# Optimization experiments

Hardware: AMD Instinct MI355X
Metric: run time of the kernel (lower is better)

Reference implementation:

```python
import jax, jax.numpy as jnp
import numpy as np

L, B, T, C, H, V = 12, 4, 1024, 768, 12, 50257
D = C // H
SCALE = 1.0 / float(np.sqrt(D))
EPS = 1e-5


def layernorm(x, g, b):
    m = jnp.mean(x, axis=-1, keepdims=True)
    v = jnp.var(x, axis=-1, keepdims=True)
    return (x - m) / jnp.sqrt(v + EPS) * g + b


def setup_inputs() -> dict:
    key = jax.random.key(0)
    ks = jax.random.split(key, 12)
    w = lambda k, shape: jax.random.normal(k, shape, jnp.float32) * 0.02
    return {
        "idx": jax.random.randint(ks[0], (B, T), 0, V),
        "tok_emb": w(ks[1], (V, C)),
        "pos_emb": w(ks[2], (1, T, C)),
        # per-layer stacked params (leading dim L); Linear stored [in, out]
        "wq": w(ks[3], (L, C, C)), "bq": jnp.zeros((L, C)),
        "wk": w(ks[4], (L, C, C)), "bk": jnp.zeros((L, C)),
        "wv": w(ks[5], (L, C, C)), "bv": jnp.zeros((L, C)),
        "wo": w(ks[6], (L, C, C)), "bo": jnp.zeros((L, C)),
        "ln1_g": jnp.ones((L, C)), "ln1_b": jnp.zeros((L, C)),
        "ln2_g": jnp.ones((L, C)), "ln2_b": jnp.zeros((L, C)),
        "w1": w(ks[7], (L, C, 4 * C)), "b1": jnp.zeros((L, 4 * C)),
        "w2": w(ks[8], (L, 4 * C, C)), "b2": jnp.zeros((L, C)),
        "lnf_g": jnp.ones((C,)), "lnf_b": jnp.zeros((C,)),
        "head_w": w(ks[9], (C, V)),
    }


def gpt_forward(idx, tok_emb, pos_emb, wq, bq, wk, bk, wv, bv, wo, bo,
                ln1_g, ln1_b, ln2_g, ln2_b, w1, b1, w2, b2,
                lnf_g, lnf_b, head_w):
    t = idx.shape[1]
    x = tok_emb[idx] + pos_emb[:, :t, :]                     # [B,T,C]
    mask = jnp.tril(jnp.ones((t, t), dtype=bool))            # causal

    def block(x, p):
        (pwq, pbq, pwk, pbk, pwv, pbv, pwo, pbo,
         g1, be1, g2, be2, pw1, pb1, pw2, pb2) = p
        h = layernorm(x, g1, be1)
        q = (h @ pwq + pbq).reshape(B, t, H, D)
        k = (h @ pwk + pbk).reshape(B, t, H, D)
        v = (h @ pwv + pbv).reshape(B, t, H, D)
        att = jnp.einsum('bthd,bshd->bhts', q, k) * SCALE    # [B,H,T,T]
        att = jnp.where(mask, att, -jnp.inf)
        att = jax.nn.softmax(att, axis=-1)
        y = jnp.einsum('bhts,bshd->bthd', att, v).reshape(B, t, C)
        x = x + y @ pwo + pbo
        h = layernorm(x, g2, be2)
        x = x + jax.nn.gelu(h @ pw1 + pb1, approximate=False) @ pw2 + pb2
        return x, None

    x, _ = jax.lax.scan(block, x, (wq, bq, wk, bk, wv, bv, wo, bo,
                                   ln1_g, ln1_b, ln2_g, ln2_b,
                                   w1, b1, w2, b2))
    x = layernorm(x, lnf_g, lnf_b)
    return x @ head_w                                        # logits [B,T,V]


def reference(idx, tok_emb, pos_emb, wq, bq, wk, bk, wv, bv, wo, bo,
              ln1_g, ln1_b, ln2_g, ln2_b, w1, b1, w2, b2,
              lnf_g, lnf_b, head_w):
    return gpt_forward(idx, tok_emb, pos_emb, wq, bq, wk, bk, wv, bv, wo, bo,
                       ln1_g, ln1_b, ln2_g, ln2_b, w1, b1, w2, b2,
                       lnf_g, lnf_b, head_w)
```

## Files before the change

### kernel.cpp

```cpp
#include <hip/hip_runtime.h>
#include <hip/hip_bf16.h>
#include <math.h>

#define L_ 12
#define B_ 4
#define T_ 1024
#define C_ 768
#define H_ 12
#define D_ 64
#define V_ 50257
#define M_ 4096
#define QKVN 2304
#define FF_ 3072
#define VPAD_ 51200

typedef __hip_bfloat16 bf16;
typedef __attribute__((ext_vector_type(4))) float f32x4;
typedef __attribute__((ext_vector_type(8))) short short8;
typedef __attribute__((ext_vector_type(8))) __bf16 bf16x8;

typedef __attribute__((address_space(1))) void gvoid;
typedef __attribute__((address_space(3))) void svoid;

__device__ __forceinline__ f32x4 mfma_bf16(short8 a, short8 b, f32x4 c) {
  return __builtin_amdgcn_mfma_f32_16x16x32_bf16(
      __builtin_bit_cast(bf16x8, a), __builtin_bit_cast(bf16x8, b), c, 0, 0, 0);
}

__device__ __forceinline__ void gload_lds16(const void* g, void* l) {
  __builtin_amdgcn_global_load_lds((gvoid*)(void*)g, (svoid*)l, 16, 0, 0);
}

__device__ __forceinline__ short f2bf(float x) {
  return __builtin_bit_cast(short, __float2bfloat16(x));
}

__global__ __launch_bounds__(256) void embed_kernel(const int* __restrict__ idx,
    const float* __restrict__ tok, const float* __restrict__ pos, float* __restrict__ x)
{
  const int row = blockIdx.x;
  const int t = row & (T_ - 1);
  const int id = idx[row];
  const float* te = tok + (size_t)id * C_;
  const float* pe = pos + (size_t)t * C_;
  float* xr = x + (size_t)row * C_;
  const int tid = threadIdx.x;
  xr[tid]       = te[tid]       + pe[tid];
  xr[tid + 256] = te[tid + 256] + pe[tid + 256];
  xr[tid + 512] = te[tid + 512] + pe[tid + 512];
}

__global__ __launch_bounds__(256) void ln_kernel(const float* __restrict__ x,
    const float* __restrict__ g, const float* __restrict__ be, bf16* __restrict__ out)
{
  const int row = blockIdx.x;
  const int tid = threadIdx.x;
  const float* xr = x + (size_t)row * C_;
  float v0 = xr[tid], v1 = xr[tid + 256], v2 = xr[tid + 512];
  float s = v0 + v1 + v2;
  float ss = v0 * v0 + v1 * v1 + v2 * v2;
#pragma unroll
  for (int o = 32; o >= 1; o >>= 1) { s += __shfl_xor(s, o, 64); ss += __shfl_xor(ss, o, 64); }
  __shared__ float sm[8];
  const int w = tid >> 6;
  if ((tid & 63) == 0) { sm[w] = s; sm[4 + w] = ss; }
  __syncthreads();
  s = sm[0] + sm[1] + sm[2] + sm[3];
  ss = sm[4] + sm[5] + sm[6] + sm[7];
  const float mean = s * (1.0f / C_);
  const float var = ss * (1.0f / C_) - mean * mean;
  const float rstd = rsqrtf(var + 1e-5f);
  bf16* orow = out + (size_t)row * C_;
  orow[tid]       = __float2bfloat16((v0 - mean) * rstd * g[tid]       + be[tid]);
  orow[tid + 256] = __float2bfloat16((v1 - mean) * rstd * g[tid + 256] + be[tid + 256]);
  orow[tid + 512] = __float2bfloat16((v2 - mean) * rstd * g[tid + 512] + be[tid + 512]);
}

__global__ __launch_bounds__(256) void convt_kernel(const float* __restrict__ in,
    bf16* __restrict__ out, int K, int N, long in_ls, long out_ls, int row_off)
{
  __shared__ float tile[64][65];
  in  += (size_t)blockIdx.z * in_ls;
  out += (size_t)blockIdx.z * out_ls;
  const int k0 = blockIdx.x * 64, n0 = blockIdx.y * 64;
  const int tid = threadIdx.x;
#pragma unroll
  for (int ph = 0; ph < 16; ph++) {
    int e = ph * 256 + tid;
    int lk = e >> 6, ln = e & 63;
    int gn = n0 + ln;
    tile[lk][ln] = (gn < N) ? in[(size_t)(k0 + lk) * N + gn] : 0.0f;
  }
  __syncthreads();
#pragma unroll
  for (int ph = 0; ph < 16; ph++) {
    int e = ph * 256 + tid;
    int lon = e >> 6, lok = e & 63;
    out[(size_t)(row_off + n0 + lon) * K + k0 + lok] = __float2bfloat16(tile[lok][lon]);
  }
}

__global__ __launch_bounds__(256) void packb_kernel(const float* __restrict__ bq,
    const float* __restrict__ bk, const float* __restrict__ bv, float* __restrict__ out)
{
  const int i = blockIdx.x * 256 + threadIdx.x;
  const int ly = i / QKVN, c = i % QKVN;
  float v;
  if (c < C_)            v = bq[ly * C_ + c];
  else if (c < 2 * C_)   v = bk[ly * C_ + c - C_];
  else                   v = bv[ly * C_ + c - 2 * C_];
  out[i] = v;
}

template<bool BIAS, bool GELU, bool RESID, bool BF16OUT>
__global__ __launch_bounds__(256) void gemm_bt(
    const short* __restrict__ A, const short* __restrict__ Bt,
    const float* __restrict__ bias, const float* resid,
    void* out, int M, int N, int K)
{
  __shared__ short As[128 * 64];
  __shared__ short Bs[128 * 64];
  const int tid = threadIdx.x;
  const int w = tid >> 6, l = tid & 63;
  const int l15 = l & 15, l4 = l >> 4;
  const int wr = w >> 1, wc = w & 1;
  const int nwg = gridDim.x * gridDim.y;
  const int id = blockIdx.y * gridDim.x + blockIdx.x;
  const int chunk = nwg >> 3;
  const int swz = (id & 7) * chunk + (id >> 3);
  const long m0 = (long)(swz % gridDim.x) * 128;
  const long n0 = (long)(swz / gridDim.x) * 128;

  f32x4 acc[4][4] = {};
  const int lrow8 = l >> 3;
  const int lc = l & 7;

  for (int kt = 0; kt < K; kt += 64) {
#pragma unroll
    for (int j = 0; j < 8; j++) {
      const int c = w * 8 + j;
      const int isA = (c < 16);
      const int cc = isA ? c : (c - 16);
      const int row = cc * 8 + lrow8;
      const int colsw = ((lc ^ (row & 7)) << 3);
      const short* gp = (isA ? A + (size_t)(m0 + row) * K : Bt + (size_t)(n0 + row) * K) + kt + colsw;
      short* sp = (isA ? As : Bs) + row * 64 + (lc << 3);
      gload_lds16(gp, sp);
    }
    __syncthreads();
#pragma unroll
    for (int ks = 0; ks < 2; ks++) {
      short8 af[4], bfr[4];
#pragma unroll
      for (int i = 0; i < 4; i++) {
        int row = wr * 64 + i * 16 + l15;
        int cs = (ks * 32 + l4 * 8) ^ ((row & 7) << 3);
        af[i] = *(const short8*)&As[row * 64 + cs];
      }
#pragma unroll
      for (int jn = 0; jn < 4; jn++) {
        int row = wc * 64 + jn * 16 + l15;
        int cs = (ks * 32 + l4 * 8) ^ ((row & 7) << 3);
        bfr[jn] = *(const short8*)&Bs[row * 64 + cs];
      }
#pragma unroll
      for (int i = 0; i < 4; i++)
#pragma unroll
        for (int jn = 0; jn < 4; jn++)
          acc[i][jn] = mfma_bf16(af[i], bfr[jn], acc[i][jn]);
    }
    __syncthreads();
  }

#pragma unroll
  for (int i = 0; i < 4; i++) {
    const long rbase = m0 + wr * 64 + i * 16 + l4 * 4;
#pragma unroll
    for (int jn = 0; jn < 4; jn++) {
      const long col = n0 + wc * 64 + jn * 16 + l15;
      const float bv = BIAS ? bias[col] : 0.0f;
#pragma unroll
      for (int r = 0; r < 4; r++) {
        float v = acc[i][jn][r] + bv;
        if (GELU) v = 0.5f * v * (1.0f + erff(v * 0.70710678118654752f));
        const size_t o = (size_t)(rbase + r) * (size_t)N + col;
        if (RESID)        ((float*)out)[o] = resid[o] + v;
        else if (BF16OUT) ((bf16*)out)[o] = __float2bfloat16(v);
        else              ((float*)out)[o] = v;
      }
    }
  }
}

template<bool BIAS, bool GELU, bool RESID, bool BF16OUT>
__global__ __launch_bounds__(256) void gemm64(
    const short* __restrict__ A, const short* __restrict__ Bt,
    const float* __restrict__ bias, const float* resid,
    void* out, int M, int N, int K)
{
  __shared__ short As[64 * 64];
  __shared__ short Bs[128 * 64];
  const int tid = threadIdx.x;
  const int w = tid >> 6, l = tid & 63;
  const int l15 = l & 15, l4 = l >> 4;
  const int wm = w >> 1, wn = w & 1;
  const int nwg = gridDim.x * gridDim.y;
  const int id = blockIdx.y * gridDim.x + blockIdx.x;
  const int chunk = nwg >> 3;
  const int swz = (id & 7) * chunk + (id >> 3);
  const long m0 = (long)(swz % gridDim.x) * 64;
  const long n0 = (long)(swz / gridDim.x) * 128;
  const int rr = tid >> 3, g = tid & 7;

  f32x4 acc[2][4] = {};

  for (int kt = 0; kt < K; kt += 64) {
#pragma unroll
    for (int p = 0; p < 2; p++) {
      const int row = p * 32 + rr;
      const int cg = ((g ^ (row & 7)) << 3);
      gload_lds16(A + (size_t)(m0 + row) * K + kt + cg, &As[row * 64 + g * 8]);
    }
#pragma unroll
    for (int p = 0; p < 4; p++) {
      const int row = p * 32 + rr;
      const int cg = ((g ^ (row & 7)) << 3);
      gload_lds16(Bt + (size_t)(n0 + row) * K + kt + cg, &Bs[row * 64 + g * 8]);
    }
    __syncthreads();
#pragma unroll
    for (int ks = 0; ks < 2; ks++) {
      short8 af[2], bfr[4];
#pragma unroll
      for (int i = 0; i < 2; i++) {
        int row = wm * 32 + i * 16 + l15;
        int cs = (ks * 32 + l4 * 8) ^ ((row & 7) << 3);
        af[i] = *(const short8*)&As[row * 64 + cs];
      }
#pragma unroll
      for (int j = 0; j < 4; j++) {
        int row = wn * 64 + j * 16 + l15;
        int cs = (ks * 32 + l4 * 8) ^ ((row & 7) << 3);
        bfr[j] = *(const short8*)&Bs[row * 64 + cs];
      }
#pragma unroll
      for (int i = 0; i < 2; i++)
#pragma unroll
        for (int j = 0; j < 4; j++)
          acc[i][j] = mfma_bf16(af[i], bfr[j], acc[i][j]);
    }
    __syncthreads();
  }

#pragma unroll
  for (int i = 0; i < 2; i++) {
    const long rbase = m0 + wm * 32 + i * 16 + l4 * 4;
#pragma unroll
    for (int j = 0; j < 4; j++) {
      const long col = n0 + wn * 64 + j * 16 + l15;
      const float bv = BIAS ? bias[col] : 0.0f;
#pragma unroll
      for (int r = 0; r < 4; r++) {
        float v = acc[i][j][r] + bv;
        if (GELU) v = 0.5f * v * (1.0f + erff(v * 0.70710678118654752f));
        const size_t o = (size_t)(rbase + r) * (size_t)N + col;
        if (RESID)        ((float*)out)[o] = resid[o] + v;
        else if (BF16OUT) ((bf16*)out)[o] = __float2bfloat16(v);
        else              ((float*)out)[o] = v;
      }
    }
  }
}

__global__ __launch_bounds__(512, 1) void gemm256(
    const short* __restrict__ A, const short* __restrict__ Bt,
    float* __restrict__ out, int N, int K)
{
  __shared__ short As[2][256 * 64];
  __shared__ short Bs[2][256 * 64];
  const int tid = threadIdx.x;
  const int l = tid & 63, l15 = l & 15, l4 = l >> 4;
  const int wv = tid >> 6, wm = wv >> 2, wn = wv & 3;
  const int bid = blockIdx.x;
  const int x = bid & 7, r = bid >> 3;
  const int mt = (x & 1) * 8 + (r & 7);
  const int nt = (x >> 1) * 50 + (r >> 3);
  const long m0 = (long)mt * 256;
  const long n0 = (long)nt * 256;
  const int nkt = K >> 6;
  const int rr = tid >> 3, g = tid & 7;

  f32x4 acc[8][4] = {};

  auto stA = [&](int s, int kt, int off) {
#pragma unroll
    for (int p = 0; p < 2; p++) {
      const int row = p * 128 + off + rr;
      gload_lds16(A + (size_t)(m0 + row) * K + (kt << 6) + ((g ^ (row & 7)) << 3),
                  &As[s][row * 64 + g * 8]);
    }
  };
  auto stB = [&](int s, int kt, int off) {
#pragma unroll
    for (int p = 0; p < 2; p++) {
      const int row = p * 128 + ((rr >> 5) << 6) + (rr & 31) + off;
      gload_lds16(Bt + (size_t)(n0 + row) * K + (kt << 6) + ((g ^ (row & 7)) << 3),
                  &Bs[s][row * 64 + g * 8]);
    }
  };
  auto rdA = [&](int s, int mf, int ks) {
    const int row = wm * 128 + mf * 16 + l15;
    const int cs = (ks * 32 + l4 * 8) ^ ((row & 7) << 3);
    return *(const short8*)&As[s][row * 64 + cs];
  };
  auto rdB = [&](int s, int nf, int ks) {
    const int row = wn * 64 + nf * 16 + l15;
    const int cs = (ks * 32 + l4 * 8) ^ ((row & 7) << 3);
    return *(const short8*)&Bs[s][row * 64 + cs];
  };

  stA(0, 0, 0); stB(0, 0, 0); stA(0, 0, 64); stB(0, 0, 32);

  int q = 0;
  for (int kt = 0; kt < nkt; ++kt, q ^= 1) {
    const int ktn = (kt + 1 < nkt) ? kt + 1 : kt;
    short8 a0[2][4], a1[2][4], b0[2][2], b1[2][2];

    stA(q ^ 1, ktn, 0);
    asm volatile("s_waitcnt vmcnt(6)" ::: "memory");
    __builtin_amdgcn_s_barrier();
#pragma unroll
    for (int ks = 0; ks < 2; ks++) {
#pragma unroll
      for (int f = 0; f < 4; f++) a0[ks][f] = rdA(q, f, ks);
#pragma unroll
      for (int j = 0; j < 2; j++) b0[ks][j] = rdB(q, j, ks);
    }
    __builtin_amdgcn_s_setprio(1);
#pragma unroll
    for (int f = 0; f < 4; f++)
#pragma unroll
      for (int j = 0; j < 2; j++) {
        acc[f][j] = mfma_bf16(a0[0][f], b0[0][j], acc[f][j]);
        acc[f][j] = mfma_bf16(a0[1][f], b0[1][j], acc[f][j]);
      }
    __builtin_amdgcn_s_setprio(0);

    stB(q ^ 1, ktn, 0);
    asm volatile("s_waitcnt vmcnt(6)" ::: "memory");
    __builtin_amdgcn_s_barrier();
#pragma unroll
    for (int ks = 0; ks < 2; ks++)
#pragma unroll
      for (int f = 0; f < 4; f++) a1[ks][f] = rdA(q, f + 4, ks);
    __builtin_amdgcn_s_setprio(1);
#pragma unroll
    for (int f = 0; f < 4; f++)
#pragma unroll
      for (int j = 0; j < 2; j++) {
        acc[f + 4][j] = mfma_bf16(a1[0][f], b0[0][j], acc[f + 4][j]);
        acc[f + 4][j] = mfma_bf16(a1[1][f], b0[1][j], acc[f + 4][j]);
      }
    __builtin_amdgcn_s_setprio(0);

    stA(q ^ 1, ktn, 64);
    asm volatile("s_waitcnt vmcnt(6)" ::: "memory");
    __builtin_amdgcn_s_barrier();
#pragma unroll
    for (int ks = 0; ks < 2; ks++)
#pragma unroll
      for (int j = 0; j < 2; j++) b1[ks][j] = rdB(q, j + 2, ks);
    __builtin_amdgcn_s_setprio(1);
#pragma unroll
    for (int f = 0; f < 4; f++)
#pragma unroll
      for (int j = 0; j < 2; j++) {
        acc[f][j + 2] = mfma_bf16(a0[0][f], b1[0][j], acc[f][j + 2]);
        acc[f][j + 2] = mfma_bf16(a0[1][f], b1[1][j], acc[f][j + 2]);
      }
    __builtin_amdgcn_s_setprio(0);

    stB(q ^ 1, ktn, 32);
    __builtin_amdgcn_s_setprio(1);
#pragma unroll
    for (int f = 0; f < 4; f++)
#pragma unroll
      for (int j = 0; j < 2; j++) {
        acc[f + 4][j + 2] = mfma_bf16(a1[0][f], b1[0][j], acc[f + 4][j + 2]);
        acc[f + 4][j + 2] = mfma_bf16(a1[1][f], b1[1][j], acc[f + 4][j + 2]);
      }
    __builtin_amdgcn_s_setprio(0);
  }

#pragma unroll
  for (int i = 0; i < 8; i++) {
#pragma unroll
    for (int j = 0; j < 4; j++) {
      const long col = n0 + wn * 64 + j * 16 + l15;
      if (col >= N) continue;
#pragma unroll
      for (int r2 = 0; r2 < 4; r2++) {
        const long row = m0 + wm * 128 + i * 16 + l4 * 4 + r2;
        out[(size_t)row * (size_t)N + col] = acc[i][j][r2];
      }
    }
  }
}

__global__ __launch_bounds__(256) void transv_kernel(const short* __restrict__ qkv,
                                                     short* __restrict__ vt)
{
  __shared__ short tile[64][72];
  const int t0 = blockIdx.x * 64, bh = blockIdx.y;
  const int b = bh / H_, h = bh % H_;
  const int tid = threadIdx.x;
#pragma unroll
  for (int ph = 0; ph < 2; ph++) {
    int lt = ph * 32 + (tid >> 3);
    int ld = (tid & 7) * 8;
    short8 v = *(const short8*)&qkv[(size_t)(b * T_ + t0 + lt) * QKVN + 2 * C_ + h * D_ + ld];
#pragma unroll
    for (int j = 0; j < 8; j++) tile[lt][ld + j] = v[j];
  }
  __syncthreads();
#pragma unroll
  for (int ph = 0; ph < 2; ph++) {
    int ldd = ph * 32 + (tid >> 3);
    int ltt = (tid & 7) * 8;
    short8 v;
#pragma unroll
    for (int j = 0; j < 8; j++) v[j] = tile[ltt + j][ldd];
    *(short8*)&vt[((size_t)bh * D_ + ldd) * T_ + t0 + ltt] = v;
  }
}

__global__ __launch_bounds__(256) void attn_kernel(const short* __restrict__ qkv,
    const short* __restrict__ vt, bf16* __restrict__ y)
{
  __shared__ short Ks[2][64 * 64];
  __shared__ short Vs[2][64 * 64];
  const int qt = (gridDim.x - 1) - blockIdx.x;
  const int bh = blockIdx.y;
  const int b = bh / H_, h = bh % H_;
  const int tid = threadIdx.x, w = tid >> 6, l = tid & 63;
  const int l15 = l & 15, l4 = l >> 4;
  const int qrow0 = qt * 64 + w * 16;
  const float SC2 = 0.125f * 1.44269504088896f;

  auto stageKV = [&](int s, int s0) {
    const short* kbase = qkv + (size_t)(b * T_ + s0) * QKVN + C_ + h * D_;
    const short* vsrc = vt + (size_t)bh * D_ * T_ + s0;
#pragma unroll
    for (int ph = 0; ph < 2; ph++) {
      int r = ph * 32 + (tid >> 3);
      int gk = ((tid & 7) ^ ((r & 3) | (((r >> 3) & 1) << 2))) << 3;
      int gv = ((tid & 7) ^ (r & 7)) << 3;
      gload_lds16(kbase + (size_t)r * QKVN + gk, &Ks[s][r * 64 + (tid & 7) * 8]);
      gload_lds16(vsrc + (size_t)r * T_ + gv, &Vs[s][r * 64 + (tid & 7) * 8]);
    }
  };

  short8 qf[2];
#pragma unroll
  for (int kf = 0; kf < 2; kf++)
    qf[kf] = *(const short8*)&qkv[(size_t)(b * T_ + qrow0 + l15) * QKVN + h * D_ + kf * 32 + l4 * 8];

  f32x4 O[4] = {};
  float mst = -1e30f, lst = 0.0f;

  stageKV(0, 0);
  __syncthreads();

  int cur = 0;
  const int qg = qrow0 + l15;
  const int send = qt * 64 + 64;
  for (int s0 = 0; s0 < send; s0 += 64) {
    if (s0 + 64 < send) stageKV(cur ^ 1, s0 + 64);
    f32x4 S[4];
#pragma unroll
    for (int c = 0; c < 4; c++) {
      const int row = 8 * (l15 >> 2) + (l15 & 3) + 4 * (c & 1) + 32 * (c >> 1);
      const int swz = (row & 3) | (((row >> 3) & 1) << 2);
      short8 k0 = *(const short8*)&Ks[cur][row * 64 + ((l4 ^ swz) << 3)];
      short8 k1 = *(const short8*)&Ks[cur][row * 64 + (((4 + l4) ^ swz) << 3)];
      f32x4 z = {0.0f, 0.0f, 0.0f, 0.0f};
      z = mfma_bf16(k0, qf[0], z);
      z = mfma_bf16(k1, qf[1], z);
      S[c] = z;
    }
#pragma unroll
    for (int c = 0; c < 4; c++) {
      const int kvb = s0 + 8 * l4 + 4 * (c & 1) + 32 * (c >> 1);
#pragma unroll
      for (int r = 0; r < 4; r++) {
        const float v = S[c][r] * SC2;
        S[c][r] = (kvb + r <= qg) ? v : -1e30f;
      }
    }
    float pm = -1e30f;
#pragma unroll
    for (int c = 0; c < 4; c++)
#pragma unroll
      for (int r = 0; r < 4; r++) pm = fmaxf(pm, S[c][r]);
    float mn;
    if (__all(pm - mst <= 8.0f)) {
      mn = mst;
    } else {
      float pm2 = fmaxf(pm, __shfl_xor(pm, 16, 64));
      pm2 = fmaxf(pm2, __shfl_xor(pm2, 32, 64));
      mn = fmaxf(mst, pm2);
      const float al = exp2f(mst - mn);
      mst = mn;
      lst *= al;
#pragma unroll
      for (int r = 0; r < 4; r++) {
        const float alr = __shfl(al, l4 * 4 + r, 16);
#pragma unroll
        for (int df = 0; df < 4; df++) O[df][r] *= alr;
      }
    }
    float rs = 0.0f;
    float pvv[4][4];
#pragma unroll
    for (int c = 0; c < 4; c++)
#pragma unroll
      for (int r = 0; r < 4; r++) { pvv[c][r] = exp2f(S[c][r] - mn); rs += pvv[c][r]; }
    rs += __shfl_xor(rs, 16, 64);
    rs += __shfl_xor(rs, 32, 64);
    lst += rs;
    short8 pa[2];
#pragma unroll
    for (int ks = 0; ks < 2; ks++)
#pragma unroll
      for (int r = 0; r < 4; r++) {
        pa[ks][r]     = f2bf(pvv[2 * ks][r]);
        pa[ks][r + 4] = f2bf(pvv[2 * ks + 1][r]);
      }
#pragma unroll
    for (int df = 0; df < 4; df++) {
      const int row = df * 16 + l15;
      short8 v0 = *(const short8*)&Vs[cur][row * 64 + ((l4 ^ (row & 7)) << 3)];
      short8 v1 = *(const short8*)&Vs[cur][row * 64 + ((((4 + l4)) ^ (row & 7)) << 3)];
      O[df] = mfma_bf16(pa[0], v0, O[df]);
      O[df] = mfma_bf16(pa[1], v1, O[df]);
    }
    __syncthreads();
    cur ^= 1;
  }

  const float inv = 1.0f / lst;
#pragma unroll
  for (int r = 0; r < 4; r++) {
    const float invr = __shfl(inv, l4 * 4 + r, 16);
    const size_t row = (size_t)(b * T_ + qrow0 + l4 * 4 + r);
#pragma unroll
    for (int df = 0; df < 4; df++)
      y[row * C_ + h * D_ + df * 16 + l15] = __float2bfloat16(O[df][r] * invr);
  }
}

extern "C" void kernel_launch(void* const* d_in, const int* in_sizes, int n_in,
                              void* d_out, int out_size, void* d_ws, size_t ws_size,
                              hipStream_t stream)
{
  const int*   idx  = (const int*)d_in[0];
  const float* tok  = (const float*)d_in[1];
  const float* pos  = (const float*)d_in[2];
  const float* wq   = (const float*)d_in[3];
  const float* bq   = (const float*)d_in[4];
  const float* wk   = (const float*)d_in[5];
  const float* bk   = (const float*)d_in[6];
  const float* wv   = (const float*)d_in[7];
  const float* bv   = (const float*)d_in[8];
  const float* wo   = (const float*)d_in[9];
  const float* bo   = (const float*)d_in[10];
  const float* ln1g = (const float*)d_in[11];
  const float* ln1b = (const float*)d_in[12];
  const float* ln2g = (const float*)d_in[13];
  const float* ln2b = (const float*)d_in[14];
  const float* w1   = (const float*)d_in[15];
  const float* b1   = (const float*)d_in[16];
  const float* w2   = (const float*)d_in[17];
  const float* b2   = (const float*)d_in[18];
  const float* lnfg = (const float*)d_in[19];
  const float* lnfb = (const float*)d_in[20];
  const float* headw= (const float*)d_in[21];

  char* p = (char*)d_ws;
  size_t off = 0;
  auto alloc = [&](size_t n) { void* r = p + off; off += (n + 255) & ~(size_t)255; return r; };
  short* qkvT  = (short*)alloc((size_t)L_ * QKVN * C_ * 2);
  short* woT   = (short*)alloc((size_t)L_ * C_ * C_ * 2);
  short* w1T   = (short*)alloc((size_t)L_ * FF_ * C_ * 2);
  short* w2T   = (short*)alloc((size_t)L_ * C_ * FF_ * 2);
  short* headT = (short*)alloc((size_t)VPAD_ * C_ * 2);
  float* qkvb  = (float*)alloc((size_t)L_ * QKVN * 4);
  float* x     = (float*)alloc((size_t)M_ * C_ * 4);
  bf16*  h     = (bf16*)alloc((size_t)M_ * C_ * 2);
  short* qkvB  = (short*)alloc((size_t)M_ * QKVN * 2);
  short* vt    = (short*)alloc((size_t)B_ * H_ * D_ * T_ * 2);
  short* y     = (short*)alloc((size_t)M_ * C_ * 2);
  short* hid   = (short*)alloc((size_t)M_ * FF_ * 2);
  if (off > ws_size) return;

  convt_kernel<<<dim3(12, 12, 12), 256, 0, stream>>>(wq, (bf16*)qkvT, C_, C_, (long)C_ * C_, (long)QKVN * C_, 0);
  convt_kernel<<<dim3(12, 12, 12), 256, 0, stream>>>(wk, (bf16*)qkvT, C_, C_, (long)C_ * C_, (long)QKVN * C_, C_);
  convt_kernel<<<dim3(12, 12, 12), 256, 0, stream>>>(wv, (bf16*)qkvT, C_, C_, (long)C_ * C_, (long)QKVN * C_, 2 * C_);
  convt_kernel<<<dim3(12, 12, 12), 256, 0, stream>>>(wo, (bf16*)woT, C_, C_, (long)C_ * C_, (long)C_ * C_, 0);
  convt_kernel<<<dim3(12, 48, 12), 256, 0, stream>>>(w1, (bf16*)w1T, C_, FF_, (long)C_ * FF_, (long)FF_ * C_, 0);
  convt_kernel<<<dim3(48, 12, 12), 256, 0, stream>>>(w2, (bf16*)w2T, FF_, C_, (long)FF_ * C_, (long)C_ * FF_, 0);
  convt_kernel<<<dim3(12, VPAD_ / 64, 1), 256, 0, stream>>>(headw, (bf16*)headT, C_, V_, 0, 0, 0);
  packb_kernel<<<dim3(108), 256, 0, stream>>>(bq, bk, bv, qkvb);

  embed_kernel<<<dim3(M_), 256, 0, stream>>>(idx, tok, pos, x);

  for (int ly = 0; ly < L_; ly++) {
    ln_kernel<<<dim3(M_), 256, 0, stream>>>(x, ln1g + ly * C_, ln1b + ly * C_, h);
    gemm_bt<true, false, false, true><<<dim3(32, 18), 256, 0, stream>>>(
        (const short*)h, qkvT + (size_t)ly * QKVN * C_, qkvb + ly * QKVN, nullptr, qkvB, M_, QKVN, C_);
    transv_kernel<<<dim3(16, 48), 256, 0, stream>>>(qkvB, vt);
    attn_kernel<<<dim3(16, 48), 256, 0, stream>>>(qkvB, vt, (bf16*)y);
    gemm64<true, false, true, false><<<dim3(64, 6), 256, 0, stream>>>(
        y, woT + (size_t)ly * C_ * C_, bo + ly * C_, x, x, M_, C_, C_);
    ln_kernel<<<dim3(M_), 256, 0, stream>>>(x, ln2g + ly * C_, ln2b + ly * C_, h);
    gemm_bt<true, true, false, true><<<dim3(32, 24), 256, 0, stream>>>(
        (const short*)h, w1T + (size_t)ly * FF_ * C_, b1 + ly * FF_, nullptr, hid, M_, FF_, C_);
    gemm64<true, false, true, false><<<dim3(64, 6), 256, 0, stream>>>(
        hid, w2T + (size_t)ly * C_ * FF_, b2 + ly * C_, x, x, M_, C_, FF_);
  }

  ln_kernel<<<dim3(M_), 256, 0, stream>>>(x, lnfg, lnfb, h);
  gemm256<<<dim3(3200), 512, 0, stream>>>((const short*)h, headT, (float*)d_out, V_, C_);
}
```

Measured before the change: 3.146 ms.

## Fuse V transpose into QKV GEMM epilogue and vectorize layernorm and weight conversion

```diff
diff --git a/kernel.cpp b/kernel.cpp
--- a/kernel.cpp
+++ b/kernel.cpp
@@ -16,6 +16,7 @@
 
 typedef __hip_bfloat16 bf16;
 typedef __attribute__((ext_vector_type(4))) float f32x4;
+typedef __attribute__((ext_vector_type(4))) short short4v;
 typedef __attribute__((ext_vector_type(8))) short short8;
 typedef __attribute__((ext_vector_type(8))) __bf16 bf16x8;
 
@@ -53,27 +54,31 @@
 __global__ __launch_bounds__(256) void ln_kernel(const float* __restrict__ x,
     const float* __restrict__ g, const float* __restrict__ be, bf16* __restrict__ out)
 {
-  const int row = blockIdx.x;
-  const int tid = threadIdx.x;
+  const int w = threadIdx.x >> 6, l = threadIdx.x & 63;
+  const int row = blockIdx.x * 4 + w;
   const float* xr = x + (size_t)row * C_;
-  float v0 = xr[tid], v1 = xr[tid + 256], v2 = xr[tid + 512];
-  float s = v0 + v1 + v2;
-  float ss = v0 * v0 + v1 * v1 + v2 * v2;
+  f32x4 v[3];
+  float s = 0.0f, ss = 0.0f;
+#pragma unroll
+  for (int p = 0; p < 3; p++) {
+    v[p] = *(const f32x4*)&xr[p * 256 + l * 4];
+#pragma unroll
+    for (int e = 0; e < 4; e++) { s += v[p][e]; ss += v[p][e] * v[p][e]; }
+  }
 #pragma unroll
   for (int o = 32; o >= 1; o >>= 1) { s += __shfl_xor(s, o, 64); ss += __shfl_xor(ss, o, 64); }
-  __shared__ float sm[8];
-  const int w = tid >> 6;
-  if ((tid & 63) == 0) { sm[w] = s; sm[4 + w] = ss; }
-  __syncthreads();
-  s = sm[0] + sm[1] + sm[2] + sm[3];
-  ss = sm[4] + sm[5] + sm[6] + sm[7];
   const float mean = s * (1.0f / C_);
-  const float var = ss * (1.0f / C_) - mean * mean;
-  const float rstd = rsqrtf(var + 1e-5f);
+  const float rstd = rsqrtf(ss * (1.0f / C_) - mean * mean + 1e-5f);
   bf16* orow = out + (size_t)row * C_;
-  orow[tid]       = __float2bfloat16((v0 - mean) * rstd * g[tid]       + be[tid]);
-  orow[tid + 256] = __float2bfloat16((v1 - mean) * rstd * g[tid + 256] + be[tid + 256]);
-  orow[tid + 512] = __float2bfloat16((v2 - mean) * rstd * g[tid + 512] + be[tid + 512]);
+#pragma unroll
+  for (int p = 0; p < 3; p++) {
+    const f32x4 gg = *(const f32x4*)&g[p * 256 + l * 4];
+    const f32x4 bb = *(const f32x4*)&be[p * 256 + l * 4];
+    short4v o4;
+#pragma unroll
+    for (int e = 0; e < 4; e++) o4[e] = f2bf((v[p][e] - mean) * rstd * gg[e] + bb[e]);
+    *(short4v*)&orow[p * 256 + l * 4] = o4;
+  }
 }
 
 __global__ __launch_bounds__(256) void convt_kernel(const float* __restrict__ in,
@@ -85,18 +90,29 @@
   const int k0 = blockIdx.x * 64, n0 = blockIdx.y * 64;
   const int tid = threadIdx.x;
 #pragma unroll
-  for (int ph = 0; ph < 16; ph++) {
-    int e = ph * 256 + tid;
-    int lk = e >> 6, ln = e & 63;
-    int gn = n0 + ln;
-    tile[lk][ln] = (gn < N) ? in[(size_t)(k0 + lk) * N + gn] : 0.0f;
+  for (int ph = 0; ph < 4; ph++) {
+    const int lk = ph * 16 + (tid >> 4);
+    const int ln = (tid & 15) * 4;
+    const int gn = n0 + ln;
+    const float* src = &in[(size_t)(k0 + lk) * N + gn];
+    f32x4 vv;
+    if (gn + 4 <= N) {
+      vv = *(const f32x4*)src;
+    } else {
+#pragma unroll
+      for (int e = 0; e < 4; e++) vv[e] = (gn + e < N) ? src[e] : 0.0f;
+    }
+    *(f32x4*)&tile[lk][ln] = vv;
   }
   __syncthreads();
 #pragma unroll
-  for (int ph = 0; ph < 16; ph++) {
-    int e = ph * 256 + tid;
-    int lon = e >> 6, lok = e & 63;
-    out[(size_t)(row_off + n0 + lon) * K + k0 + lok] = __float2bfloat16(tile[lok][lon]);
+  for (int ph = 0; ph < 2; ph++) {
+    const int lon = ph * 32 + (tid >> 3);
+    const int lok0 = (tid & 7) * 8;
+    short8 o;
+#pragma unroll
+    for (int e = 0; e < 8; e++) o[e] = f2bf(tile[lok0 + e][lon]);
+    *(short8*)&out[(size_t)(row_off + n0 + lon) * K + k0 + lok0] = o;
   }
 }
 
@@ -112,11 +128,11 @@
   out[i] = v;
 }
 
-template<bool BIAS, bool GELU, bool RESID, bool BF16OUT>
+template<bool BIAS, bool GELU, bool RESID, bool BF16OUT, bool VT>
 __global__ __launch_bounds__(256) void gemm_bt(
     const short* __restrict__ A, const short* __restrict__ Bt,
     const float* __restrict__ bias, const float* resid,
-    void* out, int M, int N, int K)
+    void* out, short* __restrict__ vt, int M, int N, int K)
 {
   __shared__ short As[128 * 64];
   __shared__ short Bs[128 * 64];
@@ -179,14 +195,24 @@
     for (int jn = 0; jn < 4; jn++) {
       const long col = n0 + wc * 64 + jn * 16 + l15;
       const float bv = BIAS ? bias[col] : 0.0f;
-#pragma unroll
-      for (int r = 0; r < 4; r++) {
-        float v = acc[i][jn][r] + bv;
-        if (GELU) v = 0.5f * v * (1.0f + erff(v * 0.70710678118654752f));
-        const size_t o = (size_t)(rbase + r) * (size_t)N + col;
-        if (RESID)        ((float*)out)[o] = resid[o] + v;
-        else if (BF16OUT) ((bf16*)out)[o] = __float2bfloat16(v);
-        else              ((float*)out)[o] = v;
+      if (VT && col >= 2 * C_) {
+        const int hd = (int)col - 2 * C_;
+        const int b = (int)(rbase >> 10);
+        const int t0 = (int)(rbase & 1023);
+        short4v o4;
+#pragma unroll
+        for (int r = 0; r < 4; r++) o4[r] = f2bf(acc[i][jn][r] + bv);
+        *(short4v*)&vt[((size_t)(b * H_) * D_ + hd) * T_ + t0] = o4;
+      } else {
+#pragma unroll
+        for (int r = 0; r < 4; r++) {
+          float v = acc[i][jn][r] + bv;
+          if (GELU) v = 0.5f * v * (1.0f + erff(v * 0.70710678118654752f));
+          const size_t o = (size_t)(rbase + r) * (size_t)N + col;
+          if (RESID)        ((float*)out)[o] = resid[o] + v;
+          else if (BF16OUT) ((bf16*)out)[o] = __float2bfloat16(v);
+          else              ((float*)out)[o] = v;
+        }
       }
     }
   }
@@ -404,33 +430,6 @@
         out[(size_t)row * (size_t)N + col] = acc[i][j][r2];
       }
     }
-  }
-}
-
-__global__ __launch_bounds__(256) void transv_kernel(const short* __restrict__ qkv,
-                                                     short* __restrict__ vt)
-{
-  __shared__ short tile[64][72];
-  const int t0 = blockIdx.x * 64, bh = blockIdx.y;
-  const int b = bh / H_, h = bh % H_;
-  const int tid = threadIdx.x;
-#pragma unroll
-  for (int ph = 0; ph < 2; ph++) {
-    int lt = ph * 32 + (tid >> 3);
-    int ld = (tid & 7) * 8;
-    short8 v = *(const short8*)&qkv[(size_t)(b * T_ + t0 + lt) * QKVN + 2 * C_ + h * D_ + ld];
-#pragma unroll
-    for (int j = 0; j < 8; j++) tile[lt][ld + j] = v[j];
-  }
-  __syncthreads();
-#pragma unroll
-  for (int ph = 0; ph < 2; ph++) {
-    int ldd = ph * 32 + (tid >> 3);
-    int ltt = (tid & 7) * 8;
-    short8 v;
-#pragma unroll
-    for (int j = 0; j < 8; j++) v[j] = tile[ltt + j][ldd];
-    *(short8*)&vt[((size_t)bh * D_ + ldd) * T_ + t0 + ltt] = v;
   }
 }
 
@@ -615,20 +614,19 @@
   embed_kernel<<<dim3(M_), 256, 0, stream>>>(idx, tok, pos, x);
 
   for (int ly = 0; ly < L_; ly++) {
-    ln_kernel<<<dim3(M_), 256, 0, stream>>>(x, ln1g + ly * C_, ln1b + ly * C_, h);
-    gemm_bt<true, false, false, true><<<dim3(32, 18), 256, 0, stream>>>(
-        (const short*)h, qkvT + (size_t)ly * QKVN * C_, qkvb + ly * QKVN, nullptr, qkvB, M_, QKVN, C_);
-    transv_kernel<<<dim3(16, 48), 256, 0, stream>>>(qkvB, vt);
+    ln_kernel<<<dim3(M_ / 4), 256, 0, stream>>>(x, ln1g + ly * C_, ln1b + ly * C_, h);
+    gemm_bt<true, false, false, true, true><<<dim3(32, 18), 256, 0, stream>>>(
+        (const short*)h, qkvT + (size_t)ly * QKVN * C_, qkvb + ly * QKVN, nullptr, qkvB, vt, M_, QKVN, C_);
     attn_kernel<<<dim3(16, 48), 256, 0, stream>>>(qkvB, vt, (bf16*)y);
     gemm64<true, false, true, false><<<dim3(64, 6), 256, 0, stream>>>(
         y, woT + (size_t)ly * C_ * C_, bo + ly * C_, x, x, M_, C_, C_);
-    ln_kernel<<<dim3(M_), 256, 0, stream>>>(x, ln2g + ly * C_, ln2b + ly * C_, h);
-    gemm_bt<true, true, false, true><<<dim3(32, 24), 256, 0, stream>>>(
-        (const short*)h, w1T + (size_t)ly * FF_ * C_, b1 + ly * FF_, nullptr, hid, M_, FF_, C_);
+    ln_kernel<<<dim3(M_ / 4), 256, 0, stream>>>(x, ln2g + ly * C_, ln2b + ly * C_, h);
+    gemm_bt<true, true, false, true, false><<<dim3(32, 24), 256, 0, stream>>>(
+        (const short*)h, w1T + (size_t)ly * FF_ * C_, b1 + ly * FF_, nullptr, hid, nullptr, M_, FF_, C_);
     gemm64<true, false, true, false><<<dim3(64, 6), 256, 0, stream>>>(
         hid, w2T + (size_t)ly * C_ * FF_, b2 + ly * C_, x, x, M_, C_, FF_);
   }
 
-  ln_kernel<<<dim3(M_), 256, 0, stream>>>(x, lnfg, lnfb, h);
+  ln_kernel<<<dim3(M_ / 4), 256, 0, stream>>>(x, lnfg, lnfb, h);
   gemm256<<<dim3(3200), 512, 0, stream>>>((const short*)h, headT, (float*)d_out, V_, C_);
 }
```

Result: faster. 3.040 ms (-3.4%).
